# Kernel optimization log

Measured on AMD Instinct MI355X. Metric: run time of the kernel, lower is better.

The kernel has to match this reference:

```python
import jax, jax.numpy as jnp
import numpy as np

D_MODEL = 1024
N_HEADS = 16
D_FF = 4096
EPS = 1e-5


def layer_norm(x, gamma, beta):
    mu = jnp.mean(x, axis=-1, keepdims=True)
    var = jnp.mean(jnp.square(x - mu), axis=-1, keepdims=True)
    return (x - mu) * jax.lax.rsqrt(var + EPS) * gamma + beta


def setup_inputs() -> dict:
    key = jax.random.key(0)
    ks = jax.random.split(key, 12)
    C, F = D_MODEL, D_FF
    s = 1.0 / np.sqrt(C)
    sf = 1.0 / np.sqrt(F)
    return {
        "src": jax.random.normal(ks[0], (2, 2048, C), dtype=jnp.float32),
        "w_qkv": jax.random.uniform(ks[1], (3 * C, C), jnp.float32, -s, s),  # qkv_bias=False
        "w_proj": jax.random.uniform(ks[2], (C, C), jnp.float32, -s, s),
        "b_proj": jax.random.uniform(ks[3], (C,), jnp.float32, -s, s),
        "w1": jax.random.uniform(ks[4], (F, C), jnp.float32, -s, s),
        "b1": jax.random.uniform(ks[5], (F,), jnp.float32, -s, s),
        "w2": jax.random.uniform(ks[6], (C, F), jnp.float32, -sf, sf),
        "b2": jax.random.uniform(ks[7], (C,), jnp.float32, -sf, sf),
        "g1": jnp.ones((C,), jnp.float32),
        "be1": jnp.zeros((C,), jnp.float32),
        "g2": jnp.ones((C,), jnp.float32),
        "be2": jnp.zeros((C,), jnp.float32),
    }


def reference(src, w_qkv, w_proj, b_proj, w1, b1, w2, b2, g1, be1, g2, be2):
    B, N, C = src.shape
    H = N_HEADS
    D = C // H
    scale = D ** -0.5
    # --- self-attention (manual QK^T softmax) ---
    qkv = (src @ w_qkv.T).reshape(B, N, 3, H, D).transpose(2, 0, 3, 1, 4)  # [3,B,H,N,D]
    q, k, v = qkv[0], qkv[1], qkv[2]
    attn = jax.nn.softmax(jnp.einsum('bhnd,bhmd->bhnm', q, k) * scale, axis=-1)
    out = jnp.einsum('bhnm,bhmd->bhnd', attn, v).transpose(0, 2, 1, 3).reshape(B, N, C)
    out = out @ w_proj.T + b_proj
    # post-norm residual
    x = layer_norm(src + out, g1, be1)
    # --- FFN ---
    ff = jax.nn.relu(x @ w1.T + b1) @ w2.T + b2
    return layer_norm(x + ff, g2, be2)
```

## Files before the change

### kernel.cpp

```cpp
#include <hip/hip_runtime.h>
#include <hip/hip_bf16.h>
#include <stdint.h>

#define TOKENS 4096
#define SEQ    2048
#define CMODEL 1024
#define HEADS  16
#define HDIM   64
#define DFF    4096
#define NT     (SEQ / 64)

typedef __attribute__((ext_vector_type(8))) short     short8;
typedef __attribute__((ext_vector_type(8))) unsigned short ushort8;
typedef __attribute__((ext_vector_type(4))) unsigned short ushort4v;
typedef __attribute__((ext_vector_type(4))) float     f32x4;

typedef const __attribute__((address_space(1))) void gbl_cvoid;
typedef __attribute__((address_space(3))) void lds_void;

__device__ inline unsigned short f2bf(float f) {
  unsigned int u = __builtin_bit_cast(unsigned int, f);
  u += 0x7fffu + ((u >> 16) & 1u);
  return (unsigned short)(u >> 16);
}
__device__ inline float bf2f(unsigned short h) {
  unsigned int u = ((unsigned int)h) << 16;
  return __builtin_bit_cast(float, u);
}

__device__ inline void gload_lds16(const unsigned short* g, unsigned short* lds) {
  __builtin_amdgcn_global_load_lds((gbl_cvoid*)g, (lds_void*)lds, 16, 0, 0);
}

#define CVT_B0 524288
#define CVT_B1 917504
#define CVT_B2 1048576
#define CVT_B3 1572864
#define CVT_B4 2097152
__global__ __launch_bounds__(256) void k_cvt_all(
    const float* __restrict__ src, const float* __restrict__ wqkv,
    const float* __restrict__ wproj, const float* __restrict__ w1,
    const float* __restrict__ w2,
    unsigned short* __restrict__ o_src, unsigned short* __restrict__ o_wqkv,
    unsigned short* __restrict__ o_wproj, unsigned short* __restrict__ o_w1,
    unsigned short* __restrict__ o_w2)
{
  const int i = blockIdx.x * 256 + threadIdx.x;
  const float* in;
  unsigned short* out;
  int off;
  if (i < CVT_B0)      { in = src;   out = o_src;   off = i; }
  else if (i < CVT_B1) { in = wqkv;  out = o_wqkv;  off = i - CVT_B0; }
  else if (i < CVT_B2) { in = wproj; out = o_wproj; off = i - CVT_B1; }
  else if (i < CVT_B3) { in = w1;    out = o_w1;    off = i - CVT_B2; }
  else                 { in = w2;    out = o_w2;    off = i - CVT_B3; }
  const float4* p = (const float4*)in + 2 * (size_t)off;
  float4 a = p[0], b = p[1];
  ushort8 o;
  o[0] = f2bf(a.x); o[1] = f2bf(a.y); o[2] = f2bf(a.z); o[3] = f2bf(a.w);
  o[4] = f2bf(b.x); o[5] = f2bf(b.y); o[6] = f2bf(b.z); o[7] = f2bf(b.w);
  ((ushort8*)out)[off] = o;
}

template<int EPI>
__global__ __launch_bounds__(256) void k_gemm_bt(
    const unsigned short* __restrict__ A,
    const unsigned short* __restrict__ B,
    unsigned short* __restrict__ Cb,
    float* __restrict__ Cf,
    const float* __restrict__ bias,
    int M, int N, int K, int kspan)
{
  __shared__ unsigned short As[3][128 * 32];
  __shared__ unsigned short Bs[3][128 * 32];
  const int t = threadIdx.x;
  const int lane = t & 63;
  const int w = t >> 6;
  const int wr = w >> 1, wc = w & 1;
  const int nwg = gridDim.x * gridDim.y;
  const int bid = blockIdx.y * gridDim.x + blockIdx.x;
  const int swz = (bid & 7) * (nwg >> 3) + (bid >> 3);
  const int n0 = (swz % gridDim.x) * 128;
  const int m0 = (swz / gridDim.x) * 128;
  const int kbase = blockIdx.z * kspan;

  const int e0 = w * 1024 + lane * 8;
  const int e1 = e0 + 512;
  const int r0 = e0 >> 5, c0 = e0 & 31;
  const int r1 = e1 >> 5, c1 = e1 & 31;

  f32x4 acc[4][4] = {};
  const int lr = lane & 15, lh = lane >> 4;
  const int nkt = kspan >> 5;

  auto stage = [&](int kt, int buf) {
    const int kb = kbase + (kt << 5);
    gload_lds16(A + (size_t)(m0 + r0) * K + kb + c0, &As[buf][w * 1024]);
    gload_lds16(A + (size_t)(m0 + r1) * K + kb + c1, &As[buf][w * 1024 + 512]);
    gload_lds16(B + (size_t)(n0 + r0) * K + kb + c0, &Bs[buf][w * 1024]);
    gload_lds16(B + (size_t)(n0 + r1) * K + kb + c1, &Bs[buf][w * 1024 + 512]);
  };
  stage(0, 0);
  if (nkt > 1) stage(1, 1);

  int buf = 0;
  for (int kt = 0; kt < nkt; ++kt) {
    if (kt + 2 < nkt) {
      const int nb = buf + 2 >= 3 ? buf - 1 : buf + 2;
      stage(kt + 2, nb);
      asm volatile("s_waitcnt vmcnt(8)" ::: "memory");
    } else if (kt + 1 < nkt) {
      asm volatile("s_waitcnt vmcnt(4)" ::: "memory");
    } else {
      asm volatile("s_waitcnt vmcnt(0)" ::: "memory");
    }
    __builtin_amdgcn_s_barrier();
    __builtin_amdgcn_sched_barrier(0);
    short8 af[4], bg[4];
#pragma unroll
    for (int m = 0; m < 4; ++m)
      af[m] = *(const short8*)&As[buf][(wr * 64 + m * 16 + lr) * 32 + lh * 8];
#pragma unroll
    for (int n = 0; n < 4; ++n)
      bg[n] = *(const short8*)&Bs[buf][(wc * 64 + n * 16 + lr) * 32 + lh * 8];
#pragma unroll
    for (int m = 0; m < 4; ++m)
#pragma unroll
      for (int n = 0; n < 4; ++n)
        acc[m][n] = __builtin_amdgcn_mfma_f32_16x16x32_bf16(af[m], bg[n], acc[m][n], 0, 0, 0);
    __builtin_amdgcn_s_barrier();
    __builtin_amdgcn_sched_barrier(0);
    buf = buf + 1 >= 3 ? 0 : buf + 1;
  }

  float* Cfp = (EPI == 4) ? Cf + (size_t)blockIdx.z * ((size_t)M * N) : Cf;
  for (int m = 0; m < 4; ++m) {
    for (int n = 0; n < 4; ++n) {
      const int col = n0 + wc * 64 + n * 16 + lr;
      for (int r = 0; r < 4; ++r) {
        const int row = m0 + wr * 64 + m * 16 + lh * 4 + r;
        const size_t idx = (size_t)row * N + col;
        float v = acc[m][n][r];
        if (EPI == 0) {
          Cb[idx] = f2bf(v);
        } else if (EPI == 2) {
          v += bias[col];
          Cb[idx] = f2bf(v > 0.f ? v : 0.f);
        } else {
          Cfp[idx] = v;
        }
      }
    }
  }
}

__global__ __launch_bounds__(256) void k_attn(
    const unsigned short* __restrict__ qkv,
    unsigned short* __restrict__ outb)
{
  __shared__ unsigned short Qs[64 * 64];
  __shared__ unsigned short Ks[2][64 * 64];
  __shared__ unsigned short Vt[2][64 * 64];
  __shared__ unsigned short Ps[4][16 * 72];

  const int t = threadIdx.x, lane = t & 63, w = t >> 6;
  const int bid0 = blockIdx.y * 32 + blockIdx.x;
  const int swz = (bid0 & 7) * 128 + (bid0 >> 3);
  const int bh = swz >> 5;
  const int b = bh >> 4, h = bh & 15;
  const int q0 = (swz & 31) * 64;
  const size_t tokbase = (size_t)b * SEQ;
  const int qoff = h * 64, koff = 1024 + h * 64, voff = 2048 + h * 64;
  const int lr = lane & 15, lh = lane >> 4, lh4 = lh * 4;

  const int srow = lane >> 3;
  const int scol = (((lane & 7) ^ srow) & 7) << 3;

  gload_lds16(qkv + (tokbase + q0 + w * 16 + srow) * 3072 + qoff + scol, &Qs[w * 1024]);
  gload_lds16(qkv + (tokbase + q0 + w * 16 + 8 + srow) * 3072 + qoff + scol, &Qs[w * 1024 + 512]);
  gload_lds16(qkv + (tokbase + w * 16 + srow) * 3072 + koff + scol, &Ks[0][w * 1024]);
  gload_lds16(qkv + (tokbase + w * 16 + 8 + srow) * 3072 + koff + scol, &Ks[0][w * 1024 + 512]);

  const int kvr = t >> 2, d0v = (t & 3) * 16;
  const int vslotbase = (t & 3) * 2, kvslot = kvr >> 3, kvlow = kvr & 7;
  const int s0v = ((kvslot ^ vslotbase) & 7) << 3;
  const int s1v = ((kvslot ^ (vslotbase + 1)) & 7) << 3;

  ushort8 vA0, vA1, vB0, vB1;
  {
    const unsigned short* vsrc = qkv + (tokbase + kvr) * 3072 + voff + d0v;
    vA0 = *(const ushort8*)vsrc;
    vA1 = *(const ushort8*)(vsrc + 8);
  }
  asm volatile("s_waitcnt vmcnt(0)" ::: "memory");
  __builtin_amdgcn_s_barrier();
  __builtin_amdgcn_sched_barrier(0);

  const int qrow = w * 16 + lr;
  const short8 aq0 = *(const short8*)&Qs[qrow * 64 + (((lh ^ (lr & 7)) & 7) << 3)];
  const short8 aq1 = *(const short8*)&Qs[qrow * 64 + ((((lh + 4) ^ (lr & 7)) & 7) << 3)];

  int koffs0[4], koffs1[4], voffs0[4], voffs1[4];
  for (int nf = 0; nf < 4; ++nf) {
    const int krow = nf * 16 + lr;
    koffs0[nf] = krow * 64 + (((lh ^ (lr & 7)) & 7) << 3);
    koffs1[nf] = krow * 64 + ((((lh + 4) ^ (lr & 7)) & 7) << 3);
    const int d = nf * 16 + lr;
    const int key = (nf * 2 + (lr >> 3)) & 7;
    voffs0[nf] = d * 64 + (((lh ^ key) & 7) << 3);
    voffs1[nf] = d * 64 + ((((lh + 4) ^ key) & 7) << 3);
  }
  const unsigned short* pa0p = &Ps[w][lr * 72 + lh * 8];
  const unsigned short* pa1p = &Ps[w][lr * 72 + 32 + lh * 8];

  float m_run = -1e30f, l_run = 0.f;
  f32x4 oacc[4] = {};
  const float SCL = 0.125f * 1.44269504089f;

#define ATTN_STEP(CUR, VA0_, VA1_, VN0_, VN1_, KT)                                \
  {                                                                               \
    const int ktn = (KT) + 1;                                                     \
    if (ktn < NT) {                                                               \
      gload_lds16(qkv + (tokbase + ktn * 64 + w * 16 + srow) * 3072 + koff + scol,\
                  &Ks[1 - (CUR)][w * 1024]);                                      \
      gload_lds16(qkv + (tokbase + ktn * 64 + w * 16 + 8 + srow) * 3072 + koff + scol,\
                  &Ks[1 - (CUR)][w * 1024 + 512]);                                \
      const unsigned short* vsrc = qkv + (tokbase + ktn * 64 + kvr) * 3072 + voff + d0v;\
      VN0_ = *(const ushort8*)vsrc;                                               \
      VN1_ = *(const ushort8*)(vsrc + 8);                                         \
      asm volatile("s_waitcnt vmcnt(4)" ::: "memory");                            \
    } else {                                                                      \
      asm volatile("s_waitcnt vmcnt(0)" ::: "memory");                            \
    }                                                                             \
    __builtin_amdgcn_s_barrier();                                                 \
    __builtin_amdgcn_sched_barrier(0);                                            \
    for (int i = 0; i < 8; ++i) Vt[CUR][(d0v + i) * 64 + s0v + kvlow] = VA0_[i];  \
    for (int i = 0; i < 8; ++i) Vt[CUR][(d0v + 8 + i) * 64 + s1v + kvlow] = VA1_[i];\
    f32x4 sacc[4] = {};                                                           \
    __builtin_amdgcn_s_setprio(1);                                                \
    for (int nf = 0; nf < 4; ++nf) {                                              \
      short8 bk0 = *(const short8*)&Ks[CUR][koffs0[nf]];                          \
      short8 bk1 = *(const short8*)&Ks[CUR][koffs1[nf]];                          \
      sacc[nf] = __builtin_amdgcn_mfma_f32_16x16x32_bf16(bk0, aq0, sacc[nf], 0, 0, 0);\
      sacc[nf] = __builtin_amdgcn_mfma_f32_16x16x32_bf16(bk1, aq1, sacc[nf], 0, 0, 0);\
    }                                                                             \
    __builtin_amdgcn_s_setprio(0);                                                \
    float a0 = fmaxf(fmaxf(sacc[0][0], sacc[0][1]), sacc[0][2]);                  \
    float a1 = fmaxf(fmaxf(sacc[0][3], sacc[1][0]), sacc[1][1]);                  \
    float a2 = fmaxf(fmaxf(sacc[1][2], sacc[1][3]), sacc[2][0]);                  \
    float a3 = fmaxf(fmaxf(sacc[2][1], sacc[2][2]), sacc[2][3]);                  \
    float a4 = fmaxf(fmaxf(sacc[3][0], sacc[3][1]), sacc[3][2]);                  \
    float tm = fmaxf(fmaxf(fmaxf(a0, a1), fmaxf(a2, a3)), fmaxf(a4, sacc[3][3])); \
    tm *= SCL;                                                                    \
    tm = fmaxf(tm, __shfl_xor(tm, 16));                                           \
    tm = fmaxf(tm, __shfl_xor(tm, 32));                                           \
    if (__any(tm > m_run + 5.f)) {               \
      const float mnew = fmaxf(m_run, tm);                                        \
      const float alpha = exp2f(m_run - mnew);                                    \
      m_run = mnew; l_run *= alpha;                                               \
      const float ar0 = __shfl(alpha, lh4 + 0), ar1 = __shfl(alpha, lh4 + 1);     \
      const float ar2 = __shfl(alpha, lh4 + 2), ar3 = __shfl(alpha, lh4 + 3);     \
      for (int nf = 0; nf < 4; ++nf) {                                            \
        oacc[nf][0] *= ar0; oacc[nf][1] *= ar1;                                   \
        oacc[nf][2] *= ar2; oacc[nf][3] *= ar3;                                   \
      }                                                                           \
    }                                                                             \
    float rs = 0.f;                                                               \
    for (int nf = 0; nf < 4; ++nf) {                                              \
      float p0 = exp2f(__builtin_fmaf(sacc[nf][0], SCL, -m_run));                 \
      float p1 = exp2f(__builtin_fmaf(sacc[nf][1], SCL, -m_run));                 \
      float p2 = exp2f(__builtin_fmaf(sacc[nf][2], SCL, -m_run));                 \
      float p3 = exp2f(__builtin_fmaf(sacc[nf][3], SCL, -m_run));                 \
      rs += (p0 + p1) + (p2 + p3);                                                \
      unsigned pk0, pk1;                                                          \
      asm("v_cvt_pk_bf16_f32 %0, %1, %2" : "=v"(pk0) : "v"(p0), "v"(p1));         \
      asm("v_cvt_pk_bf16_f32 %0, %1, %2" : "=v"(pk1) : "v"(p2), "v"(p3));         \
      uint2 pw; pw.x = pk0; pw.y = pk1;                                           \
      *(uint2*)&Ps[w][lr * 72 + nf * 16 + lh4] = pw;                              \
    }                                                                             \
    rs += __shfl_xor(rs, 16);                                                     \
    rs += __shfl_xor(rs, 32);                                                     \
    l_run += rs;                                                                  \
    short8 pa0 = *(const short8*)pa0p;                                            \
    short8 pa1 = *(const short8*)pa1p;                                            \
    asm volatile("s_waitcnt lgkmcnt(0)" ::: "memory");                            \
    __builtin_amdgcn_s_barrier();                                                 \
    __builtin_amdgcn_sched_barrier(0);                                            \
    __builtin_amdgcn_s_setprio(1);                                                \
    for (int nf = 0; nf < 4; ++nf) {                                              \
      short8 vb0 = *(const short8*)&Vt[CUR][voffs0[nf]];                          \
      short8 vb1 = *(const short8*)&Vt[CUR][voffs1[nf]];                          \
      oacc[nf] = __builtin_amdgcn_mfma_f32_16x16x32_bf16(pa0, vb0, oacc[nf], 0, 0, 0);\
      oacc[nf] = __builtin_amdgcn_mfma_f32_16x16x32_bf16(pa1, vb1, oacc[nf], 0, 0, 0);\
    }                                                                             \
    __builtin_amdgcn_s_setprio(0);                                                \
  }

  for (int kt2 = 0; kt2 < NT; kt2 += 2) {
    ATTN_STEP(0, vA0, vA1, vB0, vB1, kt2)
    ATTN_STEP(1, vB0, vB1, vA0, vA1, kt2 + 1)
  }
#undef ATTN_STEP

  const float lf0 = __shfl(l_run, lh4 + 0);
  const float lf1 = __shfl(l_run, lh4 + 1);
  const float lf2 = __shfl(l_run, lh4 + 2);
  const float lf3 = __shfl(l_run, lh4 + 3);
  const float ri0 = 1.f / lf0, ri1 = 1.f / lf1, ri2 = 1.f / lf2, ri3 = 1.f / lf3;
  for (int nf = 0; nf < 4; ++nf) {
    const int col = h * 64 + nf * 16 + lr;
    const size_t rowb = (tokbase + q0 + w * 16 + lh4) * (size_t)CMODEL + col;
    outb[rowb]               = f2bf(oacc[nf][0] * ri0);
    outb[rowb + CMODEL]      = f2bf(oacc[nf][1] * ri1);
    outb[rowb + 2 * CMODEL]  = f2bf(oacc[nf][2] * ri2);
    outb[rowb + 3 * CMODEL]  = f2bf(oacc[nf][3] * ri3);
  }
}

__global__ __launch_bounds__(256) void k_ln1(
    const float* __restrict__ p,
    const float* __restrict__ src, const float* __restrict__ bias,
    const float* __restrict__ g, const float* __restrict__ b,
    unsigned short* __restrict__ xout)
{
  const int row = blockIdx.x;
  const int t = threadIdx.x;
  const size_t rb = (size_t)row * CMODEL;
  const float4 a0 = ((const float4*)(p + rb))[t];
  const float4 a1 = ((const float4*)(p + (size_t)TOKENS * CMODEL + rb))[t];
  const float4 sv = ((const float4*)(src + rb))[t];
  const float4 bb = ((const float4*)bias)[t];
  float4 v;
  v.x = a0.x + a1.x + sv.x + bb.x;
  v.y = a0.y + a1.y + sv.y + bb.y;
  v.z = a0.z + a1.z + sv.z + bb.z;
  v.w = a0.w + a1.w + sv.w + bb.w;
  float s  = v.x + v.y + v.z + v.w;
  float s2 = v.x * v.x + v.y * v.y + v.z * v.z + v.w * v.w;
  for (int off = 32; off; off >>= 1) { s += __shfl_down(s, off); s2 += __shfl_down(s2, off); }
  __shared__ float red[8];
  __shared__ float stats[2];
  const int wv = t >> 6;
  if ((t & 63) == 0) { red[wv] = s; red[4 + wv] = s2; }
  __syncthreads();
  if (t == 0) {
    float ts  = red[0] + red[1] + red[2] + red[3];
    float ts2 = red[4] + red[5] + red[6] + red[7];
    float mu  = ts * (1.f / CMODEL);
    float var = ts2 * (1.f / CMODEL) - mu * mu;
    stats[0] = mu; stats[1] = rsqrtf(var + 1e-5f);
  }
  __syncthreads();
  const float mu = stats[0], rstd = stats[1];
  float4 gv = ((const float4*)g)[t];
  float4 bv = ((const float4*)b)[t];
  ushort4v o;
  o[0] = f2bf((v.x - mu) * rstd * gv.x + bv.x);
  o[1] = f2bf((v.y - mu) * rstd * gv.y + bv.y);
  o[2] = f2bf((v.z - mu) * rstd * gv.z + bv.z);
  o[3] = f2bf((v.w - mu) * rstd * gv.w + bv.w);
  ((ushort4v*)(xout + rb))[t] = o;
}

__global__ __launch_bounds__(256) void k_ln2(
    const float* __restrict__ q,
    const unsigned short* __restrict__ xres, const float* __restrict__ bias,
    const float* __restrict__ g, const float* __restrict__ b,
    float* __restrict__ out)
{
  const int row = blockIdx.x;
  const int t = threadIdx.x;
  const size_t rb = (size_t)row * CMODEL;
  const float4 a0 = ((const float4*)(q + rb))[t];
  const float4 a1 = ((const float4*)(q + (size_t)TOKENS * CMODEL + rb))[t];
  const ushort4v xv = ((const ushort4v*)(xres + rb))[t];
  const float4 bb = ((const float4*)bias)[t];
  float4 v;
  v.x = a0.x + a1.x + bf2f(xv[0]) + bb.x;
  v.y = a0.y + a1.y + bf2f(xv[1]) + bb.y;
  v.z = a0.z + a1.z + bf2f(xv[2]) + bb.z;
  v.w = a0.w + a1.w + bf2f(xv[3]) + bb.w;
  float s  = v.x + v.y + v.z + v.w;
  float s2 = v.x * v.x + v.y * v.y + v.z * v.z + v.w * v.w;
  for (int off = 32; off; off >>= 1) { s += __shfl_down(s, off); s2 += __shfl_down(s2, off); }
  __shared__ float red[8];
  __shared__ float stats[2];
  const int wv = t >> 6;
  if ((t & 63) == 0) { red[wv] = s; red[4 + wv] = s2; }
  __syncthreads();
  if (t == 0) {
    float ts  = red[0] + red[1] + red[2] + red[3];
    float ts2 = red[4] + red[5] + red[6] + red[7];
    float mu  = ts * (1.f / CMODEL);
    float var = ts2 * (1.f / CMODEL) - mu * mu;
    stats[0] = mu; stats[1] = rsqrtf(var + 1e-5f);
  }
  __syncthreads();
  const float mu = stats[0], rstd = stats[1];
  float4 gv = ((const float4*)g)[t];
  float4 bv = ((const float4*)b)[t];
  float4 o;
  o.x = (v.x - mu) * rstd * gv.x + bv.x;
  o.y = (v.y - mu) * rstd * gv.y + bv.y;
  o.z = (v.z - mu) * rstd * gv.z + bv.z;
  o.w = (v.w - mu) * rstd * gv.w + bv.w;
  ((float4*)(out + rb))[t] = o;
}

extern "C" void kernel_launch(void* const* d_in, const int* in_sizes, int n_in,
                              void* d_out, int out_size, void* d_ws, size_t ws_size,
                              hipStream_t stream) {
  const float* src    = (const float*)d_in[0];
  const float* w_qkv  = (const float*)d_in[1];
  const float* w_proj = (const float*)d_in[2];
  const float* b_proj = (const float*)d_in[3];
  const float* w1     = (const float*)d_in[4];
  const float* b1     = (const float*)d_in[5];
  const float* w2     = (const float*)d_in[6];
  const float* b2     = (const float*)d_in[7];
  const float* g1     = (const float*)d_in[8];
  const float* be1    = (const float*)d_in[9];
  const float* g2     = (const float*)d_in[10];
  const float* be2    = (const float*)d_in[11];
  float* out = (float*)d_out;

  char* ws = (char*)d_ws;
  size_t off = 0;
  auto alloc = [&](size_t bytes) -> void* {
    void* p = ws + off;
    off += (bytes + 255) & ~(size_t)255;
    return p;
  };
  unsigned short* src_bf   = (unsigned short*)alloc((size_t)TOKENS * CMODEL * 2);
  unsigned short* wqkv_bf  = (unsigned short*)alloc((size_t)3 * CMODEL * CMODEL * 2);
  unsigned short* wproj_bf = (unsigned short*)alloc((size_t)CMODEL * CMODEL * 2);
  unsigned short* w1_bf    = (unsigned short*)alloc((size_t)DFF * CMODEL * 2);
  unsigned short* w2_bf    = (unsigned short*)alloc((size_t)CMODEL * DFF * 2);
  unsigned short* x_bf     = (unsigned short*)alloc((size_t)TOKENS * CMODEL * 2);
  unsigned short* h_bf     = (unsigned short*)alloc((size_t)TOKENS * DFF * 2);
  char* regionR = (char*)alloc((size_t)64 * 1024 * 1024);
  unsigned short* qkv_bf   = (unsigned short*)regionR;
  unsigned short* attno_bf = (unsigned short*)(regionR + (size_t)TOKENS * 3 * CMODEL * 2);
  float*          p_proj   = (float*)(regionR + (size_t)TOKENS * 3 * CMODEL * 2 + (size_t)TOKENS * CMODEL * 2);
  float*          p_ffn2   = (float*)regionR;

  k_cvt_all<<<CVT_B4 / 256, 256, 0, stream>>>(src, w_qkv, w_proj, w1, w2,
      src_bf, wqkv_bf, wproj_bf, w1_bf, w2_bf);
  k_gemm_bt<0><<<dim3(3072 / 128, TOKENS / 128), 256, 0, stream>>>(
      src_bf, wqkv_bf, qkv_bf, nullptr, nullptr, TOKENS, 3 * CMODEL, CMODEL, CMODEL);
  k_attn<<<dim3(SEQ / 64, 2 * HEADS), 256, 0, stream>>>(qkv_bf, attno_bf);
  k_gemm_bt<4><<<dim3(CMODEL / 128, TOKENS / 128, 2), 256, 0, stream>>>(
      attno_bf, wproj_bf, nullptr, p_proj, nullptr, TOKENS, CMODEL, CMODEL, CMODEL / 2);
  k_ln1<<<TOKENS, 256, 0, stream>>>(p_proj, src, b_proj, g1, be1, x_bf);
  k_gemm_bt<2><<<dim3(DFF / 128, TOKENS / 128), 256, 0, stream>>>(
      x_bf, w1_bf, h_bf, nullptr, b1, TOKENS, DFF, CMODEL, CMODEL);
  k_gemm_bt<4><<<dim3(CMODEL / 128, TOKENS / 128, 2), 256, 0, stream>>>(
      h_bf, w2_bf, nullptr, p_ffn2, nullptr, TOKENS, CMODEL, DFF, DFF / 2);
  k_ln2<<<TOKENS, 256, 0, stream>>>(p_ffn2, x_bf, b2, g2, be2, out);
}
```

Measured before the change: 393.3 us.

## Produce V transposed from a separate GEMM and async-load it into attention LDS

The QKV projection is split into a Q/K GEMM and a second GEMM that writes V already transposed (head-dim major, token minor). The attention kernel can then fill its V tile in LDS with the same async global-to-LDS loads and swizzle it uses for K, replacing the per-thread register loads and scalar LDS transpose stores. One of the two barriers per step is also removed. The cost is an extra kernel launch and a V GEMM with a different grid shape, plus the risk that the reordered barrier leaves a race on the double-buffered tiles.

```diff
diff --git a/kernel.cpp b/kernel.cpp
--- a/kernel.cpp
+++ b/kernel.cpp
@@ -155,7 +155,8 @@
 }
 
 __global__ __launch_bounds__(256) void k_attn(
-    const unsigned short* __restrict__ qkv,
+    const unsigned short* __restrict__ qk,
+    const unsigned short* __restrict__ vT,
     unsigned short* __restrict__ outb)
 {
   __shared__ unsigned short Qs[64 * 64];
@@ -170,28 +171,19 @@
   const int b = bh >> 4, h = bh & 15;
   const int q0 = (swz & 31) * 64;
   const size_t tokbase = (size_t)b * SEQ;
-  const int qoff = h * 64, koff = 1024 + h * 64, voff = 2048 + h * 64;
+  const int qoff = h * 64, koff = 1024 + h * 64;
+  const size_t vbase = (size_t)(h * 64) * TOKENS + tokbase;
   const int lr = lane & 15, lh = lane >> 4, lh4 = lh * 4;
 
   const int srow = lane >> 3;
   const int scol = (((lane & 7) ^ srow) & 7) << 3;
 
-  gload_lds16(qkv + (tokbase + q0 + w * 16 + srow) * 3072 + qoff + scol, &Qs[w * 1024]);
-  gload_lds16(qkv + (tokbase + q0 + w * 16 + 8 + srow) * 3072 + qoff + scol, &Qs[w * 1024 + 512]);
-  gload_lds16(qkv + (tokbase + w * 16 + srow) * 3072 + koff + scol, &Ks[0][w * 1024]);
-  gload_lds16(qkv + (tokbase + w * 16 + 8 + srow) * 3072 + koff + scol, &Ks[0][w * 1024 + 512]);
-
-  const int kvr = t >> 2, d0v = (t & 3) * 16;
-  const int vslotbase = (t & 3) * 2, kvslot = kvr >> 3, kvlow = kvr & 7;
-  const int s0v = ((kvslot ^ vslotbase) & 7) << 3;
-  const int s1v = ((kvslot ^ (vslotbase + 1)) & 7) << 3;
-
-  ushort8 vA0, vA1, vB0, vB1;
-  {
-    const unsigned short* vsrc = qkv + (tokbase + kvr) * 3072 + voff + d0v;
-    vA0 = *(const ushort8*)vsrc;
-    vA1 = *(const ushort8*)(vsrc + 8);
-  }
+  gload_lds16(qk + (tokbase + q0 + w * 16 + srow) * 2048 + qoff + scol, &Qs[w * 1024]);
+  gload_lds16(qk + (tokbase + q0 + w * 16 + 8 + srow) * 2048 + qoff + scol, &Qs[w * 1024 + 512]);
+  gload_lds16(qk + (tokbase + w * 16 + srow) * 2048 + koff + scol, &Ks[0][w * 1024]);
+  gload_lds16(qk + (tokbase + w * 16 + 8 + srow) * 2048 + koff + scol, &Ks[0][w * 1024 + 512]);
+  gload_lds16(vT + vbase + (size_t)(w * 16 + srow) * TOKENS + scol, &Vt[0][w * 1024]);
+  gload_lds16(vT + vbase + (size_t)(w * 16 + 8 + srow) * TOKENS + scol, &Vt[0][w * 1024 + 512]);
   asm volatile("s_waitcnt vmcnt(0)" ::: "memory");
   __builtin_amdgcn_s_barrier();
   __builtin_amdgcn_sched_barrier(0);
@@ -205,10 +197,8 @@
     const int krow = nf * 16 + lr;
     koffs0[nf] = krow * 64 + (((lh ^ (lr & 7)) & 7) << 3);
     koffs1[nf] = krow * 64 + ((((lh + 4) ^ (lr & 7)) & 7) << 3);
-    const int d = nf * 16 + lr;
-    const int key = (nf * 2 + (lr >> 3)) & 7;
-    voffs0[nf] = d * 64 + (((lh ^ key) & 7) << 3);
-    voffs1[nf] = d * 64 + ((((lh + 4) ^ key) & 7) << 3);
+    voffs0[nf] = koffs0[nf];
+    voffs1[nf] = koffs1[nf];
   }
   const unsigned short* pa0p = &Ps[w][lr * 72 + lh * 8];
   const unsigned short* pa1p = &Ps[w][lr * 72 + 32 + lh * 8];
@@ -217,25 +207,24 @@
   f32x4 oacc[4] = {};
   const float SCL = 0.125f * 1.44269504089f;
 
-#define ATTN_STEP(CUR, VA0_, VA1_, VN0_, VN1_, KT)                                \
+#define ATTN_STEP(CUR, KT)                                                        \
   {                                                                               \
     const int ktn = (KT) + 1;                                                     \
     if (ktn < NT) {                                                               \
-      gload_lds16(qkv + (tokbase + ktn * 64 + w * 16 + srow) * 3072 + koff + scol,\
+      gload_lds16(qk + (tokbase + ktn * 64 + w * 16 + srow) * 2048 + koff + scol, \
                   &Ks[1 - (CUR)][w * 1024]);                                      \
-      gload_lds16(qkv + (tokbase + ktn * 64 + w * 16 + 8 + srow) * 3072 + koff + scol,\
+      gload_lds16(qk + (tokbase + ktn * 64 + w * 16 + 8 + srow) * 2048 + koff + scol,\
                   &Ks[1 - (CUR)][w * 1024 + 512]);                                \
-      const unsigned short* vsrc = qkv + (tokbase + ktn * 64 + kvr) * 3072 + voff + d0v;\
-      VN0_ = *(const ushort8*)vsrc;                                               \
-      VN1_ = *(const ushort8*)(vsrc + 8);                                         \
+      gload_lds16(vT + vbase + ktn * 64 + (size_t)(w * 16 + srow) * TOKENS + scol,\
+                  &Vt[1 - (CUR)][w * 1024]);                                      \
+      gload_lds16(vT + vbase + ktn * 64 + (size_t)(w * 16 + 8 + srow) * TOKENS + scol,\
+                  &Vt[1 - (CUR)][w * 1024 + 512]);                                \
       asm volatile("s_waitcnt vmcnt(4)" ::: "memory");                            \
     } else {                                                                      \
       asm volatile("s_waitcnt vmcnt(0)" ::: "memory");                            \
     }                                                                             \
     __builtin_amdgcn_s_barrier();                                                 \
     __builtin_amdgcn_sched_barrier(0);                                            \
-    for (int i = 0; i < 8; ++i) Vt[CUR][(d0v + i) * 64 + s0v + kvlow] = VA0_[i];  \
-    for (int i = 0; i < 8; ++i) Vt[CUR][(d0v + 8 + i) * 64 + s1v + kvlow] = VA1_[i];\
     f32x4 sacc[4] = {};                                                           \
     __builtin_amdgcn_s_setprio(1);                                                \
     for (int nf = 0; nf < 4; ++nf) {                                              \
@@ -283,9 +272,6 @@
     l_run += rs;                                                                  \
     short8 pa0 = *(const short8*)pa0p;                                            \
     short8 pa1 = *(const short8*)pa1p;                                            \
-    asm volatile("s_waitcnt lgkmcnt(0)" ::: "memory");                            \
-    __builtin_amdgcn_s_barrier();                                                 \
-    __builtin_amdgcn_sched_barrier(0);                                            \
     __builtin_amdgcn_s_setprio(1);                                                \
     for (int nf = 0; nf < 4; ++nf) {                                              \
       short8 vb0 = *(const short8*)&Vt[CUR][voffs0[nf]];                          \
@@ -294,11 +280,13 @@
       oacc[nf] = __builtin_amdgcn_mfma_f32_16x16x32_bf16(pa1, vb1, oacc[nf], 0, 0, 0);\
     }                                                                             \
     __builtin_amdgcn_s_setprio(0);                                                \
+    __builtin_amdgcn_s_barrier();            \
+    __builtin_amdgcn_sched_barrier(0);                                            \
   }
 
   for (int kt2 = 0; kt2 < NT; kt2 += 2) {
-    ATTN_STEP(0, vA0, vA1, vB0, vB1, kt2)
-    ATTN_STEP(1, vB0, vB1, vA0, vA1, kt2 + 1)
+    ATTN_STEP(0, kt2)
+    ATTN_STEP(1, kt2 + 1)
   }
 #undef ATTN_STEP
 
@@ -439,16 +427,23 @@
   unsigned short* x_bf     = (unsigned short*)alloc((size_t)TOKENS * CMODEL * 2);
   unsigned short* h_bf     = (unsigned short*)alloc((size_t)TOKENS * DFF * 2);
   char* regionR = (char*)alloc((size_t)64 * 1024 * 1024);
-  unsigned short* qkv_bf   = (unsigned short*)regionR;
-  unsigned short* attno_bf = (unsigned short*)(regionR + (size_t)TOKENS * 3 * CMODEL * 2);
-  float*          p_proj   = (float*)(regionR + (size_t)TOKENS * 3 * CMODEL * 2 + (size_t)TOKENS * CMODEL * 2);
+  unsigned short* qk_bf    = (unsigned short*)regionR;
+  unsigned short* vT_bf    = (unsigned short*)(regionR + (size_t)TOKENS * 2048 * 2);
+  unsigned short* attno_bf = (unsigned short*)(regionR + (size_t)TOKENS * 2048 * 2
+                                                       + (size_t)CMODEL * TOKENS * 2);
+  float*          p_proj   = (float*)(regionR + (size_t)TOKENS * 2048 * 2
+                                              + (size_t)CMODEL * TOKENS * 2
+                                              + (size_t)TOKENS * CMODEL * 2);
   float*          p_ffn2   = (float*)regionR;
 
   k_cvt_all<<<CVT_B4 / 256, 256, 0, stream>>>(src, w_qkv, w_proj, w1, w2,
       src_bf, wqkv_bf, wproj_bf, w1_bf, w2_bf);
-  k_gemm_bt<0><<<dim3(3072 / 128, TOKENS / 128), 256, 0, stream>>>(
-      src_bf, wqkv_bf, qkv_bf, nullptr, nullptr, TOKENS, 3 * CMODEL, CMODEL, CMODEL);
-  k_attn<<<dim3(SEQ / 64, 2 * HEADS), 256, 0, stream>>>(qkv_bf, attno_bf);
+  k_gemm_bt<0><<<dim3(2048 / 128, TOKENS / 128), 256, 0, stream>>>(
+      src_bf, wqkv_bf, qk_bf, nullptr, nullptr, TOKENS, 2048, CMODEL, CMODEL);
+  k_gemm_bt<0><<<dim3(TOKENS / 128, CMODEL / 128), 256, 0, stream>>>(
+      wqkv_bf + (size_t)2048 * CMODEL, src_bf, vT_bf, nullptr, nullptr,
+      CMODEL, TOKENS, CMODEL, CMODEL);
+  k_attn<<<dim3(SEQ / 64, 2 * HEADS), 256, 0, stream>>>(qk_bf, vT_bf, attno_bf);
   k_gemm_bt<4><<<dim3(CMODEL / 128, TOKENS / 128, 2), 256, 0, stream>>>(
       attno_bf, wproj_bf, nullptr, p_proj, nullptr, TOKENS, CMODEL, CMODEL, CMODEL / 2);
   k_ln1<<<TOKENS, 256, 0, stream>>>(p_proj, src, b_proj, g1, be1, x_bf);
```

New measurement: 400.7 us. Within noise of the previous version (+1.9%).
